# Performance work log

Measured on AMD Instinct MI355X. Metric: run time of the kernel, lower is better.

Reference implementation:

```python
import jax, jax.numpy as jnp
import numpy as np
from jax import lax

B, S, W = 64, 64, 12          # batch, sentences, words-per-sentence (max_seq)
V, SYM, HID = 32000, 128, 256  # vocab, symbol_size, hidden_size
E, R = 64, 32                  # entity_size, role_size
EPS = 1e-5


def _mlp(x, W1, b1, W2, b2):
    # equation 'b...e,er->b...r' is a matmul on the last axis; tanh hidden, linear out
    return jnp.tanh(x @ W1 + b1) @ W2 + b2


def _ln(x, g, b):
    mu = jnp.mean(x, axis=-1, keepdims=True)
    var = jnp.mean(jnp.square(x - mu), axis=-1, keepdims=True)
    return (x - mu) * lax.rsqrt(var + EPS) * g + b


def setup_inputs() -> dict:
    key = jax.random.key(0)
    ks = jax.random.split(key, 24)
    s_in = 1.0 / np.sqrt(SYM)
    s_h = 1.0 / np.sqrt(HID)
    inp = {
        "story": jax.random.randint(ks[0], (B, S, W), 0, V),
        "query": jax.random.randint(ks[1], (B, W), 0, V),
        "word_embed": jax.random.uniform(ks[2], (V, SYM), jnp.float32, -0.1, 0.1),
        "pos_embed": jnp.ones((W, SYM), jnp.float32) / W,
        # UpdateModule MLPs: 2 entity heads (out=E), 3 role heads (out=R), stacked
        "ue_W1": jax.random.normal(ks[3], (2, SYM, HID)) * s_in,
        "ue_b1": jnp.zeros((2, HID), jnp.float32),
        "ue_W2": jax.random.normal(ks[4], (2, HID, E)) * s_h,
        "ue_b2": jnp.zeros((2, E), jnp.float32),
        "ur_W1": jax.random.normal(ks[5], (3, SYM, HID)) * s_in,
        "ur_b1": jnp.zeros((3, HID), jnp.float32),
        "ur_W2": jax.random.normal(ks[6], (3, HID, R)) * s_h,
        "ur_b2": jnp.zeros((3, R), jnp.float32),
        # InferenceModule MLPs
        "ie_W1": jax.random.normal(ks[7], (2, SYM, HID)) * s_in,
        "ie_b1": jnp.zeros((2, HID), jnp.float32),
        "ie_W2": jax.random.normal(ks[8], (2, HID, E)) * s_h,
        "ie_b2": jnp.zeros((2, E), jnp.float32),
        "ir_W1": jax.random.normal(ks[9], (3, SYM, HID)) * s_in,
        "ir_b1": jnp.zeros((3, HID), jnp.float32),
        "ir_W2": jax.random.normal(ks[10], (3, HID, R)) * s_h,
        "ir_b2": jnp.zeros((3, R), jnp.float32),
        "ln_g": jnp.ones((3, E), jnp.float32),
        "ln_b": jnp.zeros((3, E), jnp.float32),
        "Z": jax.random.normal(ks[11], (E, V)) * (1.0 / np.sqrt(E)),
    }
    return inp


def reference(story, query, word_embed, pos_embed,
              ue_W1, ue_b1, ue_W2, ue_b2, ur_W1, ur_b1, ur_W2, ur_b2,
              ie_W1, ie_b1, ie_W2, ie_b2, ir_W1, ir_b1, ir_W2, ir_b2,
              ln_g, ln_b, Z):
    # ---- InputModule ----
    sent = jnp.einsum('bswe,we->bse', word_embed[story], pos_embed)   # [B,S,SYM]
    qsum = jnp.einsum('bwe,we->be', word_embed[query], pos_embed)     # [B,SYM]

    # ---- UpdateModule: precompute per-step entity/role vectors ----
    e1 = _mlp(sent, ue_W1[0], ue_b1[0], ue_W2[0], ue_b2[0])  # [B,S,E]
    e2 = _mlp(sent, ue_W1[1], ue_b1[1], ue_W2[1], ue_b2[1])
    r1 = _mlp(sent, ur_W1[0], ur_b1[0], ur_W2[0], ur_b2[0])  # [B,S,R]
    r2 = _mlp(sent, ur_W1[1], ur_b1[1], ur_W2[1], ur_b2[1])
    r3 = _mlp(sent, ur_W1[2], ur_b1[2], ur_W2[2], ur_b2[2])
    paW = jnp.einsum('bsr,bsf->bsrf', r1, e2)
    paB = jnp.einsum('bsr,bsf->bsrf', r3, e1)

    xs = tuple(jnp.moveaxis(t, 1, 0) for t in (e1, r1, paW, e2, r2, paB, r3))

    def step(TPR, x):
        e1i, r1i, paWi, e2i, r2i, paBi, r3i = x
        t1 = jnp.einsum('be,berf->brf', e1i, TPR)
        w_hat = jnp.einsum('br,brf->bf', r1i, t1)
        m_hat = jnp.einsum('br,brf->bf', r2i, t1)
        b_hat = jnp.einsum('be,br,berf->bf', e2i, r3i, TPR)
        write_op = paWi - r1i[:, :, None] * w_hat[:, None, :]
        move_op = r2i[:, :, None] * (w_hat - m_hat)[:, None, :]
        back_op = paBi - r3i[:, :, None] * b_hat[:, None, :]
        delta = (jnp.einsum('be,brf->berf', e1i, write_op + move_op)
                 + jnp.einsum('be,brf->berf', e2i, back_op))
        return TPR + delta, None

    TPR0 = jnp.zeros((sent.shape[0], E, R, E), sent.dtype)
    TPR, _ = lax.scan(step, TPR0, xs)

    # ---- InferenceModule ----
    qe1 = _mlp(qsum, ie_W1[0], ie_b1[0], ie_W2[0], ie_b2[0])
    qr1 = _mlp(qsum, ir_W1[0], ir_b1[0], ir_W2[0], ir_b2[0])
    qr2 = _mlp(qsum, ir_W1[1], ir_b1[1], ir_W2[1], ir_b2[1])
    qr3 = _mlp(qsum, ir_W1[2], ir_b1[2], ir_W2[2], ir_b2[2])
    i1 = _ln(jnp.einsum('be,br,berf->bf', qe1, qr1, TPR), ln_g[0], ln_b[0])
    i2 = _ln(jnp.einsum('be,br,berf->bf', i1, qr2, TPR), ln_g[1], ln_b[1])
    i3 = _ln(jnp.einsum('be,br,berf->bf', i2, qr3, TPR), ln_g[2], ln_b[2])
    return (i1 + i2 + i3) @ Z
```

## Files before the change

kernel.cpp:

```cpp
#include <hip/hip_runtime.h>
#include <math.h>

#define B_   64
#define S_   64
#define W_   12
#define V_   32000
#define SYM_ 128
#define HID_ 256
#define E_   64
#define R_   32

__global__ __launch_bounds__(128) void k_embed(
    const int* __restrict__ story, const int* __restrict__ query,
    const float* __restrict__ we, const float* __restrict__ pe,
    float* __restrict__ X) {
  int row = blockIdx.x;
  int e = threadIdx.x;
  const int* idx = (row < 4096) ? story + row * W_ : query + (row - 4096) * W_;
  float acc = 0.f;
#pragma unroll
  for (int w = 0; w < W_; ++w)
    acc = fmaf(we[(long)idx[w] * SYM_ + e], pe[w * SYM_ + e], acc);
  X[row * SYM_ + e] = acc;
}

__global__ __launch_bounds__(256) void k_mlp(
    const float* __restrict__ X,
    const float* __restrict__ ueW1, const float* __restrict__ ueb1,
    const float* __restrict__ ueW2, const float* __restrict__ ueb2,
    const float* __restrict__ urW1, const float* __restrict__ urb1,
    const float* __restrict__ urW2, const float* __restrict__ urb2,
    const float* __restrict__ ieW1, const float* __restrict__ ieb1,
    const float* __restrict__ ieW2, const float* __restrict__ ieb2,
    const float* __restrict__ irW1, const float* __restrict__ irb1,
    const float* __restrict__ irW2, const float* __restrict__ irb2,
    float* __restrict__ oE0, float* __restrict__ oE1,
    float* __restrict__ oR0, float* __restrict__ oR1, float* __restrict__ oR2) {
  __shared__ float SM[8320];

  int h = blockIdx.x % 5;
  int tile = blockIdx.x / 5;
  int rowbase = tile * 32;
  bool isQ = (rowbase >= 4096);
  bool isE = (h < 2);
  const float* W1 = isE ? (isQ ? ieW1 : ueW1) + h * (SYM_ * HID_)
                        : (isQ ? irW1 : urW1) + (h - 2) * (SYM_ * HID_);
  const float* b1 = isE ? (isQ ? ieb1 : ueb1) + h * HID_
                        : (isQ ? irb1 : urb1) + (h - 2) * HID_;
  const float* W2 = isE ? (isQ ? ieW2 : ueW2) + h * (HID_ * E_)
                        : (isQ ? irW2 : urW2) + (h - 2) * (HID_ * R_);
  const float* b2 = isE ? (isQ ? ieb2 : ueb2) + h * E_
                        : (isQ ? irb2 : urb2) + (h - 2) * R_;
  float* out = (h == 0) ? oE0 : (h == 1) ? oE1 : (h == 2) ? oR0 : (h == 3) ? oR1 : oR2;

  int tid = threadIdx.x;
  int wv = tid >> 6;
  int l = tid & 63;

#pragma unroll
  for (int c = 0; c < 4; ++c) {
    int i = tid + 256 * c;
    int row = i >> 5, k4 = (i & 31) * 4;
    *(float4*)&SM[row * 136 + k4] = *(const float4*)(X + (long)(rowbase + row) * SYM_ + k4);
  }
  __syncthreads();

  float a[8][4];
#pragma unroll
  for (int i = 0; i < 8; ++i)
#pragma unroll
    for (int q = 0; q < 4; ++q) a[i][q] = 0.f;

  const float* W1p = W1 + 4 * l;
#pragma unroll 2
  for (int kg = 0; kg < 32; ++kg) {
    float4 w0 = *(const float4*)(W1p + (long)(4 * kg + 0) * HID_);
    float4 w1 = *(const float4*)(W1p + (long)(4 * kg + 1) * HID_);
    float4 w2 = *(const float4*)(W1p + (long)(4 * kg + 2) * HID_);
    float4 w3 = *(const float4*)(W1p + (long)(4 * kg + 3) * HID_);
    float4 xr[8];
#pragma unroll
    for (int i = 0; i < 8; ++i)
      xr[i] = *(const float4*)&SM[(8 * wv + i) * 136 + 4 * kg];
#pragma unroll
    for (int i = 0; i < 8; ++i) {
      a[i][0] = fmaf(xr[i].x, w0.x, a[i][0]);
      a[i][1] = fmaf(xr[i].x, w0.y, a[i][1]);
      a[i][2] = fmaf(xr[i].x, w0.z, a[i][2]);
      a[i][3] = fmaf(xr[i].x, w0.w, a[i][3]);
      a[i][0] = fmaf(xr[i].y, w1.x, a[i][0]);
      a[i][1] = fmaf(xr[i].y, w1.y, a[i][1]);
      a[i][2] = fmaf(xr[i].y, w1.z, a[i][2]);
      a[i][3] = fmaf(xr[i].y, w1.w, a[i][3]);
      a[i][0] = fmaf(xr[i].z, w2.x, a[i][0]);
      a[i][1] = fmaf(xr[i].z, w2.y, a[i][1]);
      a[i][2] = fmaf(xr[i].z, w2.z, a[i][2]);
      a[i][3] = fmaf(xr[i].z, w2.w, a[i][3]);
      a[i][0] = fmaf(xr[i].w, w3.x, a[i][0]);
      a[i][1] = fmaf(xr[i].w, w3.y, a[i][1]);
      a[i][2] = fmaf(xr[i].w, w3.z, a[i][2]);
      a[i][3] = fmaf(xr[i].w, w3.w, a[i][3]);
    }
  }
  __syncthreads();
  {
    float4 b1v = *(const float4*)(b1 + 4 * l);
#pragma unroll
    for (int i = 0; i < 8; ++i) {
      float4 hv = make_float4(tanhf(a[i][0] + b1v.x), tanhf(a[i][1] + b1v.y),
                              tanhf(a[i][2] + b1v.z), tanhf(a[i][3] + b1v.w));
      *(float4*)&SM[(8 * wv + i) * 260 + 4 * l] = hv;
    }
  }
  __syncthreads();
  if (isE) {
    float acc[8];
#pragma unroll
    for (int i = 0; i < 8; ++i) acc[i] = 0.f;
#pragma unroll 2
    for (int c4 = 0; c4 < 64; ++c4) {
      float w0 = W2[(long)(4 * c4 + 0) * E_ + l];
      float w1 = W2[(long)(4 * c4 + 1) * E_ + l];
      float w2 = W2[(long)(4 * c4 + 2) * E_ + l];
      float w3 = W2[(long)(4 * c4 + 3) * E_ + l];
#pragma unroll
      for (int i = 0; i < 8; ++i) {
        float4 hh = *(const float4*)&SM[(8 * wv + i) * 260 + 4 * c4];
        acc[i] = fmaf(hh.x, w0, fmaf(hh.y, w1, fmaf(hh.z, w2, fmaf(hh.w, w3, acc[i]))));
      }
    }
    float bb = b2[l];
#pragma unroll
    for (int i = 0; i < 8; ++i)
      out[(long)(rowbase + 8 * wv + i) * E_ + l] = acc[i] + bb;
  } else {
    int lc = l & 31;
    float acc[8];
#pragma unroll
    for (int i = 0; i < 8; ++i) acc[i] = 0.f;
#pragma unroll 2
    for (int c4 = 0; c4 < 64; ++c4) {
      float w0 = W2[(long)(4 * c4 + 0) * R_ + lc];
      float w1 = W2[(long)(4 * c4 + 1) * R_ + lc];
      float w2 = W2[(long)(4 * c4 + 2) * R_ + lc];
      float w3 = W2[(long)(4 * c4 + 3) * R_ + lc];
#pragma unroll
      for (int i = 0; i < 8; ++i) {
        float4 hh = *(const float4*)&SM[(8 * wv + i) * 260 + 4 * c4];
        acc[i] = fmaf(hh.x, w0, fmaf(hh.y, w1, fmaf(hh.z, w2, fmaf(hh.w, w3, acc[i]))));
      }
    }
    if (l < 32) {
      float bb = b2[lc];
#pragma unroll
      for (int i = 0; i < 8; ++i)
        out[(long)(rowbase + 8 * wv + i) * R_ + lc] = acc[i] + bb;
    }
  }
}

__global__ __launch_bounds__(256) void k_gram(
    const float* __restrict__ e1, const float* __restrict__ e2,
    const float* __restrict__ r1, const float* __restrict__ r2,
    const float* __restrict__ r3, float* __restrict__ Wt) {
  int b = blockIdx.x / 9, m = blockIdx.x % 9;
  const float* sE = ((m < 6) ? e1 : e2) + (long)b * S_ * E_;
  const float* jE = ((m == 2 || m == 5 || m == 8) ? e2 : e1) + (long)b * S_ * E_;
  int sk = m / 3, jk = m % 3;
  const float* sR = ((sk == 0) ? r1 : (sk == 1) ? r2 : r3) + (long)b * S_ * R_;
  const float* jR = ((jk == 0) ? r1 : (jk == 1) ? r2 : r3) + (long)b * S_ * R_;

  __shared__ float Es[64][68], Ej[64][68], Rs[64][36], Rj[64][36];
  int tid = threadIdx.x;
  for (int i = tid; i < 1024; i += 256) {
    int row = i >> 4, c = i & 15;
    *(float4*)&Es[row][4 * c] = *(const float4*)(sE + row * 64 + 4 * c);
    *(float4*)&Ej[row][4 * c] = *(const float4*)(jE + row * 64 + 4 * c);
  }
  for (int i = tid; i < 512; i += 256) {
    int row = i >> 3, c = i & 7;
    *(float4*)&Rs[row][4 * c] = *(const float4*)(sR + row * 32 + 4 * c);
    *(float4*)&Rj[row][4 * c] = *(const float4*)(jR + row * 32 + 4 * c);
  }
  __syncthreads();

  int s0 = (tid & 15) * 4, j0 = (tid >> 4) * 4;
  float ed[4][4] = {}, rd[4][4] = {};
#pragma unroll 4
  for (int k = 0; k < 16; ++k) {
    float4 es[4], ej[4];
#pragma unroll
    for (int i = 0; i < 4; ++i) {
      es[i] = *(const float4*)&Es[s0 + i][4 * k];
      ej[i] = *(const float4*)&Ej[j0 + i][4 * k];
    }
#pragma unroll
    for (int i = 0; i < 4; ++i)
#pragma unroll
      for (int j = 0; j < 4; ++j)
        ed[i][j] = fmaf(es[i].x, ej[j].x, fmaf(es[i].y, ej[j].y,
                   fmaf(es[i].z, ej[j].z, fmaf(es[i].w, ej[j].w, ed[i][j]))));
  }
#pragma unroll 4
  for (int k = 0; k < 8; ++k) {
    float4 rs[4], rj[4];
#pragma unroll
    for (int i = 0; i < 4; ++i) {
      rs[i] = *(const float4*)&Rs[s0 + i][4 * k];
      rj[i] = *(const float4*)&Rj[j0 + i][4 * k];
    }
#pragma unroll
    for (int i = 0; i < 4; ++i)
#pragma unroll
      for (int j = 0; j < 4; ++j)
        rd[i][j] = fmaf(rs[i].x, rj[j].x, fmaf(rs[i].y, rj[j].y,
                   fmaf(rs[i].z, rj[j].z, fmaf(rs[i].w, rj[j].w, rd[i][j]))));
  }
  float* wout = Wt + (long)(b * 9 + m) * 4096;
#pragma unroll
  for (int jj = 0; jj < 4; ++jj) {
    float4 o4 = make_float4(ed[0][jj] * rd[0][jj], ed[1][jj] * rd[1][jj],
                            ed[2][jj] * rd[2][jj], ed[3][jj] * rd[3][jj]);
    *(float4*)(wout + (j0 + jj) * 64 + s0) = o4;
  }
}

__global__ __launch_bounds__(256) void k_scan(
    const float* __restrict__ e1g, const float* __restrict__ e2g,
    const float* __restrict__ Wt, float4* __restrict__ acd) {
  __shared__ float WtL[9 * 512];
  int b = blockIdx.x & 63;
  int g = blockIdx.x >> 6;
  int tid = threadIdx.x;
  int wv = tid >> 6;
  int lane = tid & 63;
  int f0 = g * 8 + wv * 2;
  int f1 = f0 + 1;
  const float* Wb = Wt + (long)b * 9 * 4096;
  long eoff = ((long)b * 64 + lane) * 64;
  float e1x = e1g[eoff + f0], e1y = e1g[eoff + f1];
  float e2x = e2g[eoff + f0], e2y = e2g[eoff + f1];

  float pW0 = 0.f, pM0 = 0.f, pB0 = 0.f;
  float pW1 = 0.f, pM1 = 0.f, pB1 = 0.f;
  float ca0 = e2x, cc0 = 0.f, cd0 = e1x;
  float ca1 = e2y, cc1 = 0.f, cd1 = e1y;
  float ka0 = 0.f, kc0 = 0.f, kd0 = 0.f;
  float ka1 = 0.f, kc1 = 0.f, kd1 = 0.f;

  for (int jc = 0; jc < 8; ++jc) {
    __syncthreads();
    for (int i = tid; i < 1152; i += 256) {
      int m = i >> 7;
      int off = (i & 127) * 4;
      *(float4*)&WtL[m * 512 + off] = *(const float4*)(Wb + m * 4096 + jc * 512 + off);
    }
    __syncthreads();
#pragma unroll
    for (int jj = 0; jj < 8; ++jj) {
      int j = jc * 8 + jj;
      float wa = WtL[0 * 512 + jj * 64 + lane];
      float wc = WtL[1 * 512 + jj * 64 + lane];
      float wd = WtL[2 * 512 + jj * 64 + lane];
      float ma = WtL[3 * 512 + jj * 64 + lane];
      float mc = WtL[4 * 512 + jj * 64 + lane];
      float md = WtL[5 * 512 + jj * 64 + lane];
      float ba = WtL[6 * 512 + jj * 64 + lane];
      float bc = WtL[7 * 512 + jj * 64 + lane];
      float bd = WtL[8 * 512 + jj * 64 + lane];
      float aj0 = __int_as_float(__builtin_amdgcn_readlane(__float_as_int(ca0), j));
      float cj0 = __int_as_float(__builtin_amdgcn_readlane(__float_as_int(cc0), j));
      float dj0 = __int_as_float(__builtin_amdgcn_readlane(__float_as_int(cd0), j));
      float aj1 = __int_as_float(__builtin_amdgcn_readlane(__float_as_int(ca1), j));
      float cj1 = __int_as_float(__builtin_amdgcn_readlane(__float_as_int(cc1), j));
      float dj1 = __int_as_float(__builtin_amdgcn_readlane(__float_as_int(cd1), j));
      bool own = (lane == j);
      ka0 = own ? ca0 : ka0; kc0 = own ? cc0 : kc0; kd0 = own ? cd0 : kd0;
      ka1 = own ? ca1 : ka1; kc1 = own ? cc1 : kc1; kd1 = own ? cd1 : kd1;
      pW0 = fmaf(wa, aj0, pW0); pW0 = fmaf(wc, cj0, pW0); pW0 = fmaf(wd, dj0, pW0);
      pM0 = fmaf(ma, aj0, pM0); pM0 = fmaf(mc, cj0, pM0); pM0 = fmaf(md, dj0, pM0);
      pB0 = fmaf(ba, aj0, pB0); pB0 = fmaf(bc, cj0, pB0); pB0 = fmaf(bd, dj0, pB0);
      pW1 = fmaf(wa, aj1, pW1); pW1 = fmaf(wc, cj1, pW1); pW1 = fmaf(wd, dj1, pW1);
      pM1 = fmaf(ma, aj1, pM1); pM1 = fmaf(mc, cj1, pM1); pM1 = fmaf(md, dj1, pM1);
      pB1 = fmaf(ba, aj1, pB1); pB1 = fmaf(bc, cj1, pB1); pB1 = fmaf(bd, dj1, pB1);
      ca0 = e2x - pW0; cc0 = pW0 - pM0; cd0 = e1x - pB0;
      ca1 = e2y - pW1; cc1 = pW1 - pM1; cd1 = e1y - pB1;
    }
  }
  acd[eoff + f0] = make_float4(ka0, kc0, kd0, 0.f);
  acd[eoff + f1] = make_float4(ka1, kc1, kd1, 0.f);
}

__global__ __launch_bounds__(1024) void k_infer(
    const float4* __restrict__ acd,
    const float* __restrict__ e1, const float* __restrict__ e2,
    const float* __restrict__ r1, const float* __restrict__ r2,
    const float* __restrict__ r3,
    const float* __restrict__ qe1, const float* __restrict__ qr1,
    const float* __restrict__ qr2, const float* __restrict__ qr3,
    const float* __restrict__ lng, const float* __restrict__ lnb,
    float* __restrict__ isum) {
  int b = blockIdx.x, tid = threadIdx.x;
  __shared__ float hista[64 * 65], histc[64 * 65], histd[64 * 65];
  __shared__ float vlds[9 * 64];
  __shared__ float ivec[64];
  __shared__ float u1s[64], u2s[64];
  __shared__ float dsc[64];

  {
    const float4* ab = acd + (long)b * 4096;
    for (int idx = tid; idx < 4096; idx += 1024) {
      float4 hv = ab[idx];
      int j = idx >> 6, f = idx & 63;
      hista[j * 65 + f] = hv.x;
      histc[j * 65 + f] = hv.y;
      histd[j * 65 + f] = hv.z;
    }
  }
  if (tid < 576) {
    int pk = tid >> 6, j = tid & 63;
    int p = pk / 3, k = pk % 3;
    const float* rv = ((k == 0) ? r1 : (k == 1) ? r2 : r3) + ((long)b * 64 + j) * 32;
    const float* q = ((p == 0) ? qr1 : (p == 1) ? qr2 : qr3) + b * 32;
    float acc = 0.f;
#pragma unroll
    for (int t = 0; t < 8; ++t) {
      float4 rv4 = *(const float4*)(rv + 4 * t);
      float4 q4 = *(const float4*)(q + 4 * t);
      acc = fmaf(rv4.x, q4.x, fmaf(rv4.y, q4.y,
            fmaf(rv4.z, q4.z, fmaf(rv4.w, q4.w, acc))));
    }
    vlds[pk * 64 + j] = acc;
  }
  if (tid < 64) ivec[tid] = qe1[b * 64 + tid];
  __syncthreads();

  int f = tid >> 4, jsl = tid & 15;
  int dotd = tid >> 3, dt = tid & 7;
  int which = dotd >> 6, dj = dotd & 63;
  const float* erow = (which ? e2 : e1) + ((long)b * 64 + dj) * 64 + dt * 8;
  float isacc = 0.f;
  for (int p = 0; p < 3; ++p) {
    {
      float acc = 0.f;
#pragma unroll
      for (int t = 0; t < 8; ++t)
        acc = fmaf(erow[t], ivec[dt * 8 + t], acc);
      acc += __shfl_xor(acc, 1, 64);
      acc += __shfl_xor(acc, 2, 64);
      acc += __shfl_xor(acc, 4, 64);
      if (dt == 0) { if (which) u2s[dj] = acc; else u1s[dj] = acc; }
    }
    __syncthreads();
    float part = 0.f;
#pragma unroll
    for (int i = 0; i < 4; ++i) {
      int j = jsl * 4 + i;
      float ca = u1s[j] * vlds[(p * 3 + 0) * 64 + j];
      float cc = u1s[j] * vlds[(p * 3 + 1) * 64 + j];
      float cd = u2s[j] * vlds[(p * 3 + 2) * 64 + j];
      part = fmaf(ca, hista[j * 65 + f],
             fmaf(cc, histc[j * 65 + f],
             fmaf(cd, histd[j * 65 + f], part)));
    }
    part += __shfl_xor(part, 1, 64);
    part += __shfl_xor(part, 2, 64);
    part += __shfl_xor(part, 4, 64);
    part += __shfl_xor(part, 8, 64);
    if (jsl == 0) dsc[f] = part;
    __syncthreads();
    if (tid < 64) {
      float v = dsc[tid];
      float mu = v;
#pragma unroll
      for (int mm = 1; mm <= 32; mm <<= 1) mu += __shfl_xor(mu, mm, 64);
      mu *= (1.f / 64.f);
      float d = v - mu;
      float vr = d * d;
#pragma unroll
      for (int mm = 1; mm <= 32; mm <<= 1) vr += __shfl_xor(vr, mm, 64);
      vr *= (1.f / 64.f);
      float iv = d * (1.f / sqrtf(vr + 1e-5f)) * lng[p * 64 + tid] + lnb[p * 64 + tid];
      ivec[tid] = iv;
      isacc += iv;
    }
    __syncthreads();
  }
  if (tid < 64) isum[b * 64 + tid] = isacc;
}

__global__ __launch_bounds__(256) void k_final(
    const float* __restrict__ isum, const float* __restrict__ Zm,
    float* __restrict__ out) {
  __shared__ float isT[64 * 68];
  int tid = threadIdx.x;
  for (int i = tid; i < 4096; i += 256) {
    int bb = i >> 6, e = i & 63;
    isT[e * 68 + bb] = isum[i];
  }
  __syncthreads();
  int tr = tid >> 4, tc = tid & 15;
  int v0 = blockIdx.x * 64 + tc * 4;
  float acc[4][4] = {};
#pragma unroll 2
  for (int e = 0; e < 64; ++e) {
    float4 a4 = *(const float4*)&isT[e * 68 + 4 * tr];
    float4 z4 = *(const float4*)(Zm + (long)e * V_ + v0);
    float as[4] = {a4.x, a4.y, a4.z, a4.w};
    float zs[4] = {z4.x, z4.y, z4.z, z4.w};
#pragma unroll
    for (int i = 0; i < 4; ++i)
#pragma unroll
      for (int j = 0; j < 4; ++j) acc[i][j] = fmaf(as[i], zs[j], acc[i][j]);
  }
#pragma unroll
  for (int i = 0; i < 4; ++i) {
    float4 o4 = make_float4(acc[i][0], acc[i][1], acc[i][2], acc[i][3]);
    *(float4*)(out + (long)(4 * tr + i) * V_ + v0) = o4;
  }
}

extern "C" void kernel_launch(void* const* d_in, const int* in_sizes, int n_in,
                              void* d_out, int out_size, void* d_ws, size_t ws_size,
                              hipStream_t stream) {
  const int* story = (const int*)d_in[0];
  const int* query = (const int*)d_in[1];
  const float* we = (const float*)d_in[2];
  const float* pe = (const float*)d_in[3];
  const float* ueW1 = (const float*)d_in[4];
  const float* ueb1 = (const float*)d_in[5];
  const float* ueW2 = (const float*)d_in[6];
  const float* ueb2 = (const float*)d_in[7];
  const float* urW1 = (const float*)d_in[8];
  const float* urb1 = (const float*)d_in[9];
  const float* urW2 = (const float*)d_in[10];
  const float* urb2 = (const float*)d_in[11];
  const float* ieW1 = (const float*)d_in[12];
  const float* ieb1 = (const float*)d_in[13];
  const float* ieW2 = (const float*)d_in[14];
  const float* ieb2 = (const float*)d_in[15];
  const float* irW1 = (const float*)d_in[16];
  const float* irb1 = (const float*)d_in[17];
  const float* irW2 = (const float*)d_in[18];
  const float* irb2 = (const float*)d_in[19];
  const float* lng = (const float*)d_in[20];
  const float* lnb = (const float*)d_in[21];
  const float* Zm = (const float*)d_in[22];

  float* ws = (float*)d_ws;
  float* X = ws;
  float* e1 = X + 532480;
  float* e2 = e1 + 266240;
  float* r1 = e2 + 266240;
  float* r2 = r1 + 133120;
  float* r3 = r2 + 133120;
  float* isum = r3 + 133120;
  float* Wt = isum + 4096;
  float4* acd = (float4*)(Wt + 2359296);
  float* qe1 = e1 + 4096 * 64;
  float* qr1 = r1 + 4096 * 32;
  float* qr2 = r2 + 4096 * 32;
  float* qr3 = r3 + 4096 * 32;
  float* outF = (float*)d_out;

  k_embed<<<4160, 128, 0, stream>>>(story, query, we, pe, X);
  k_mlp<<<130 * 5, 256, 0, stream>>>(X, ueW1, ueb1, ueW2, ueb2,
                                     urW1, urb1, urW2, urb2,
                                     ieW1, ieb1, ieW2, ieb2,
                                     irW1, irb1, irW2, irb2,
                                     e1, e2, r1, r2, r3);
  k_gram<<<64 * 9, 256, 0, stream>>>(e1, e2, r1, r2, r3, Wt);
  k_scan<<<512, 256, 0, stream>>>(e1, e2, Wt, acd);
  k_infer<<<B_, 1024, 0, stream>>>(acd, e1, e2, r1, r2, r3, qe1, qr1, qr2, qr3,
                                   lng, lnb, isum);
  k_final<<<V_ / 64, 256, 0, stream>>>(isum, Zm, outF);
}
```

Baseline: 220.6 us.

## Drop LDS staging in MLP, scan and infer kernels; read directly from global

```diff
diff --git a/kernel.cpp b/kernel.cpp
--- a/kernel.cpp
+++ b/kernel.cpp
@@ -36,7 +36,7 @@
     const float* __restrict__ irW2, const float* __restrict__ irb2,
     float* __restrict__ oE0, float* __restrict__ oE1,
     float* __restrict__ oR0, float* __restrict__ oR1, float* __restrict__ oR2) {
-  __shared__ float SM[8320];
+  __shared__ float HT[32 * 260];
 
   int h = blockIdx.x % 5;
   int tile = blockIdx.x / 5;
@@ -57,14 +57,6 @@
   int wv = tid >> 6;
   int l = tid & 63;
 
-#pragma unroll
-  for (int c = 0; c < 4; ++c) {
-    int i = tid + 256 * c;
-    int row = i >> 5, k4 = (i & 31) * 4;
-    *(float4*)&SM[row * 136 + k4] = *(const float4*)(X + (long)(rowbase + row) * SYM_ + k4);
-  }
-  __syncthreads();
-
   float a[8][4];
 #pragma unroll
   for (int i = 0; i < 8; ++i)
@@ -72,6 +64,7 @@
     for (int q = 0; q < 4; ++q) a[i][q] = 0.f;
 
   const float* W1p = W1 + 4 * l;
+  const float* Xw = X + (long)(rowbase + 8 * wv) * SYM_;
 #pragma unroll 2
   for (int kg = 0; kg < 32; ++kg) {
     float4 w0 = *(const float4*)(W1p + (long)(4 * kg + 0) * HID_);
@@ -81,7 +74,7 @@
     float4 xr[8];
 #pragma unroll
     for (int i = 0; i < 8; ++i)
-      xr[i] = *(const float4*)&SM[(8 * wv + i) * 136 + 4 * kg];
+      xr[i] = *(const float4*)(Xw + i * SYM_ + 4 * kg);
 #pragma unroll
     for (int i = 0; i < 8; ++i) {
       a[i][0] = fmaf(xr[i].x, w0.x, a[i][0]);
@@ -102,14 +95,13 @@
       a[i][3] = fmaf(xr[i].w, w3.w, a[i][3]);
     }
   }
-  __syncthreads();
   {
     float4 b1v = *(const float4*)(b1 + 4 * l);
 #pragma unroll
     for (int i = 0; i < 8; ++i) {
       float4 hv = make_float4(tanhf(a[i][0] + b1v.x), tanhf(a[i][1] + b1v.y),
                               tanhf(a[i][2] + b1v.z), tanhf(a[i][3] + b1v.w));
-      *(float4*)&SM[(8 * wv + i) * 260 + 4 * l] = hv;
+      *(float4*)&HT[(8 * wv + i) * 260 + 4 * l] = hv;
     }
   }
   __syncthreads();
@@ -125,7 +117,7 @@
       float w3 = W2[(long)(4 * c4 + 3) * E_ + l];
 #pragma unroll
       for (int i = 0; i < 8; ++i) {
-        float4 hh = *(const float4*)&SM[(8 * wv + i) * 260 + 4 * c4];
+        float4 hh = *(const float4*)&HT[(8 * wv + i) * 260 + 4 * c4];
         acc[i] = fmaf(hh.x, w0, fmaf(hh.y, w1, fmaf(hh.z, w2, fmaf(hh.w, w3, acc[i]))));
       }
     }
@@ -134,10 +126,9 @@
     for (int i = 0; i < 8; ++i)
       out[(long)(rowbase + 8 * wv + i) * E_ + l] = acc[i] + bb;
   } else {
-    int lc = l & 31;
-    float acc[8];
-#pragma unroll
-    for (int i = 0; i < 8; ++i) acc[i] = 0.f;
+    int h2 = l >> 5, lc = l & 31;
+    int rA = 8 * wv + 4 * h2;
+    float acc[4] = {};
 #pragma unroll 2
     for (int c4 = 0; c4 < 64; ++c4) {
       float w0 = W2[(long)(4 * c4 + 0) * R_ + lc];
@@ -145,17 +136,15 @@
       float w2 = W2[(long)(4 * c4 + 2) * R_ + lc];
       float w3 = W2[(long)(4 * c4 + 3) * R_ + lc];
 #pragma unroll
-      for (int i = 0; i < 8; ++i) {
-        float4 hh = *(const float4*)&SM[(8 * wv + i) * 260 + 4 * c4];
+      for (int i = 0; i < 4; ++i) {
+        float4 hh = *(const float4*)&HT[(rA + i) * 260 + 4 * c4];
         acc[i] = fmaf(hh.x, w0, fmaf(hh.y, w1, fmaf(hh.z, w2, fmaf(hh.w, w3, acc[i]))));
       }
     }
-    if (l < 32) {
-      float bb = b2[lc];
-#pragma unroll
-      for (int i = 0; i < 8; ++i)
-        out[(long)(rowbase + 8 * wv + i) * R_ + lc] = acc[i] + bb;
-    }
+    float bb = b2[lc];
+#pragma unroll
+    for (int i = 0; i < 4; ++i)
+      out[(long)(rowbase + rA + i) * R_ + lc] = acc[i] + bb;
   }
 }
 
@@ -228,7 +217,6 @@
 __global__ __launch_bounds__(256) void k_scan(
     const float* __restrict__ e1g, const float* __restrict__ e2g,
     const float* __restrict__ Wt, float4* __restrict__ acd) {
-  __shared__ float WtL[9 * 512];
   int b = blockIdx.x & 63;
   int g = blockIdx.x >> 6;
   int tid = threadIdx.x;
@@ -236,7 +224,7 @@
   int lane = tid & 63;
   int f0 = g * 8 + wv * 2;
   int f1 = f0 + 1;
-  const float* Wb = Wt + (long)b * 9 * 4096;
+  const float* Wb = Wt + (long)b * 9 * 4096 + lane;
   long eoff = ((long)b * 64 + lane) * 64;
   float e1x = e1g[eoff + f0], e1y = e1g[eoff + f1];
   float e2x = e2g[eoff + f0], e2y = e2g[eoff + f1];
@@ -248,26 +236,16 @@
   float ka0 = 0.f, kc0 = 0.f, kd0 = 0.f;
   float ka1 = 0.f, kc1 = 0.f, kd1 = 0.f;
 
-  for (int jc = 0; jc < 8; ++jc) {
-    __syncthreads();
-    for (int i = tid; i < 1152; i += 256) {
-      int m = i >> 7;
-      int off = (i & 127) * 4;
-      *(float4*)&WtL[m * 512 + off] = *(const float4*)(Wb + m * 4096 + jc * 512 + off);
-    }
-    __syncthreads();
-#pragma unroll
-    for (int jj = 0; jj < 8; ++jj) {
-      int j = jc * 8 + jj;
-      float wa = WtL[0 * 512 + jj * 64 + lane];
-      float wc = WtL[1 * 512 + jj * 64 + lane];
-      float wd = WtL[2 * 512 + jj * 64 + lane];
-      float ma = WtL[3 * 512 + jj * 64 + lane];
-      float mc = WtL[4 * 512 + jj * 64 + lane];
-      float md = WtL[5 * 512 + jj * 64 + lane];
-      float ba = WtL[6 * 512 + jj * 64 + lane];
-      float bc = WtL[7 * 512 + jj * 64 + lane];
-      float bd = WtL[8 * 512 + jj * 64 + lane];
+  for (int j0 = 0; j0 < 64; j0 += 4) {
+    float w[9][4];
+#pragma unroll
+    for (int m = 0; m < 9; ++m)
+#pragma unroll
+      for (int jj = 0; jj < 4; ++jj)
+        w[m][jj] = Wb[m * 4096 + (j0 + jj) * 64];
+#pragma unroll
+    for (int jj = 0; jj < 4; ++jj) {
+      int j = j0 + jj;
       float aj0 = __int_as_float(__builtin_amdgcn_readlane(__float_as_int(ca0), j));
       float cj0 = __int_as_float(__builtin_amdgcn_readlane(__float_as_int(cc0), j));
       float dj0 = __int_as_float(__builtin_amdgcn_readlane(__float_as_int(cd0), j));
@@ -277,12 +255,12 @@
       bool own = (lane == j);
       ka0 = own ? ca0 : ka0; kc0 = own ? cc0 : kc0; kd0 = own ? cd0 : kd0;
       ka1 = own ? ca1 : ka1; kc1 = own ? cc1 : kc1; kd1 = own ? cd1 : kd1;
-      pW0 = fmaf(wa, aj0, pW0); pW0 = fmaf(wc, cj0, pW0); pW0 = fmaf(wd, dj0, pW0);
-      pM0 = fmaf(ma, aj0, pM0); pM0 = fmaf(mc, cj0, pM0); pM0 = fmaf(md, dj0, pM0);
-      pB0 = fmaf(ba, aj0, pB0); pB0 = fmaf(bc, cj0, pB0); pB0 = fmaf(bd, dj0, pB0);
-      pW1 = fmaf(wa, aj1, pW1); pW1 = fmaf(wc, cj1, pW1); pW1 = fmaf(wd, dj1, pW1);
-      pM1 = fmaf(ma, aj1, pM1); pM1 = fmaf(mc, cj1, pM1); pM1 = fmaf(md, dj1, pM1);
-      pB1 = fmaf(ba, aj1, pB1); pB1 = fmaf(bc, cj1, pB1); pB1 = fmaf(bd, dj1, pB1);
+      pW0 = fmaf(w[0][jj], aj0, pW0); pW0 = fmaf(w[1][jj], cj0, pW0); pW0 = fmaf(w[2][jj], dj0, pW0);
+      pM0 = fmaf(w[3][jj], aj0, pM0); pM0 = fmaf(w[4][jj], cj0, pM0); pM0 = fmaf(w[5][jj], dj0, pM0);
+      pB0 = fmaf(w[6][jj], aj0, pB0); pB0 = fmaf(w[7][jj], cj0, pB0); pB0 = fmaf(w[8][jj], dj0, pB0);
+      pW1 = fmaf(w[0][jj], aj1, pW1); pW1 = fmaf(w[1][jj], cj1, pW1); pW1 = fmaf(w[2][jj], dj1, pW1);
+      pM1 = fmaf(w[3][jj], aj1, pM1); pM1 = fmaf(w[4][jj], cj1, pM1); pM1 = fmaf(w[5][jj], dj1, pM1);
+      pB1 = fmaf(w[6][jj], aj1, pB1); pB1 = fmaf(w[7][jj], cj1, pB1); pB1 = fmaf(w[8][jj], dj1, pB1);
       ca0 = e2x - pW0; cc0 = pW0 - pM0; cd0 = e1x - pB0;
       ca1 = e2y - pW1; cc1 = pW1 - pM1; cd1 = e1y - pB1;
     }
@@ -301,22 +279,13 @@
     const float* __restrict__ lng, const float* __restrict__ lnb,
     float* __restrict__ isum) {
   int b = blockIdx.x, tid = threadIdx.x;
-  __shared__ float hista[64 * 65], histc[64 * 65], histd[64 * 65];
   __shared__ float vlds[9 * 64];
   __shared__ float ivec[64];
   __shared__ float u1s[64], u2s[64];
+  __shared__ float part[16 * 64];
   __shared__ float dsc[64];
-
-  {
-    const float4* ab = acd + (long)b * 4096;
-    for (int idx = tid; idx < 4096; idx += 1024) {
-      float4 hv = ab[idx];
-      int j = idx >> 6, f = idx & 63;
-      hista[j * 65 + f] = hv.x;
-      histc[j * 65 + f] = hv.y;
-      histd[j * 65 + f] = hv.z;
-    }
-  }
+  const float4* ab = acd + (long)b * 4096;
+
   if (tid < 576) {
     int pk = tid >> 6, j = tid & 63;
     int p = pk / 3, k = pk % 3;
@@ -335,7 +304,7 @@
   if (tid < 64) ivec[tid] = qe1[b * 64 + tid];
   __syncthreads();
 
-  int f = tid >> 4, jsl = tid & 15;
+  int f = tid & 63, jg = tid >> 6;
   int dotd = tid >> 3, dt = tid & 7;
   int which = dotd >> 6, dj = dotd & 63;
   const float* erow = (which ? e2 : e1) + ((long)b * 64 + dj) * 64 + dt * 8;
@@ -352,25 +321,22 @@
       if (dt == 0) { if (which) u2s[dj] = acc; else u1s[dj] = acc; }
     }
     __syncthreads();
-    float part = 0.f;
+    float pt = 0.f;
 #pragma unroll
     for (int i = 0; i < 4; ++i) {
-      int j = jsl * 4 + i;
+      int j = jg * 4 + i;
+      float4 hv = ab[j * 64 + f];
       float ca = u1s[j] * vlds[(p * 3 + 0) * 64 + j];
       float cc = u1s[j] * vlds[(p * 3 + 1) * 64 + j];
       float cd = u2s[j] * vlds[(p * 3 + 2) * 64 + j];
-      part = fmaf(ca, hista[j * 65 + f],
-             fmaf(cc, histc[j * 65 + f],
-             fmaf(cd, histd[j * 65 + f], part)));
-    }
-    part += __shfl_xor(part, 1, 64);
-    part += __shfl_xor(part, 2, 64);
-    part += __shfl_xor(part, 4, 64);
-    part += __shfl_xor(part, 8, 64);
-    if (jsl == 0) dsc[f] = part;
+      pt = fmaf(ca, hv.x, fmaf(cc, hv.y, fmaf(cd, hv.z, pt)));
+    }
+    part[jg * 64 + f] = pt;
     __syncthreads();
     if (tid < 64) {
-      float v = dsc[tid];
+      float v = 0.f;
+#pragma unroll
+      for (int g2 = 0; g2 < 16; ++g2) v += part[g2 * 64 + tid];
       float mu = v;
 #pragma unroll
       for (int mm = 1; mm <= 32; mm <<= 1) mu += __shfl_xor(mu, mm, 64);
```

Result: slower. 232.0 us (+5.2%).
